# Performance work log

Measured on AMD Instinct MI355X. Metric: run time of the kernel, lower is better.

## Reference

```python
import jax, jax.numpy as jnp
import numpy as np
from functools import partial

P = 14          # patch size
IMG = 448       # image size
D = 1152        # hidden dim
H = 16          # num heads
DH = D // H     # head dim = 72
I = 4304        # intermediate dim
L = 4           # num layers
N = (IMG // P) ** 2  # 1024 patches
EPS = 1e-6


def setup_inputs() -> dict:
    key = jax.random.key(0)
    ks = jax.random.split(key, 24)
    s = 0.02
    inp = {
        "images": jax.random.normal(ks[0], (2, 2, IMG, IMG, 3), jnp.float32),
        "conv_w": jax.random.normal(ks[1], (P, P, 3, D), jnp.float32) * s,
        "conv_b": jnp.zeros((D,), jnp.float32),
        "pos_emb": jax.random.normal(ks[2], (N, D), jnp.float32) * s,
        # per-layer stacked parameters, leading axis L
        "ln1_g": jnp.ones((L, D), jnp.float32),
        "ln1_b": jnp.zeros((L, D), jnp.float32),
        "Wq": jax.random.normal(ks[3], (L, D, D), jnp.float32) * s,
        "bq": jnp.zeros((L, D), jnp.float32),
        "Wk": jax.random.normal(ks[4], (L, D, D), jnp.float32) * s,
        "bk": jnp.zeros((L, D), jnp.float32),
        "Wv": jax.random.normal(ks[5], (L, D, D), jnp.float32) * s,
        "bv": jnp.zeros((L, D), jnp.float32),
        "Wo": jax.random.normal(ks[6], (L, D, D), jnp.float32) * s,
        "bo": jnp.zeros((L, D), jnp.float32),
        "ln2_g": jnp.ones((L, D), jnp.float32),
        "ln2_b": jnp.zeros((L, D), jnp.float32),
        "W1": jax.random.normal(ks[7], (L, D, I), jnp.float32) * s,
        "b1": jnp.zeros((L, I), jnp.float32),
        "W2": jax.random.normal(ks[8], (L, I, D), jnp.float32) * s,
        "b2": jnp.zeros((L, D), jnp.float32),
        "lnf_g": jnp.ones((D,), jnp.float32),
        "lnf_b": jnp.zeros((D,), jnp.float32),
    }
    return inp


def _layernorm(x, g, b):
    mu = jnp.mean(x, axis=-1, keepdims=True)
    var = jnp.var(x, axis=-1, keepdims=True)
    return (x - mu) * jax.lax.rsqrt(var + EPS) * g + b


def _encoder(images, conv_w, conv_b, pos_emb, ln1_g, ln1_b, Wq, bq, Wk, bk,
             Wv, bv, Wo, bo, ln2_g, ln2_b, W1, b1, W2, b2, lnf_g, lnf_b):
    B, T = images.shape[0], images.shape[1]
    x = images.reshape((B * T,) + images.shape[2:])  # [BT, IMG, IMG, 3]
    # patch embedding: Conv2D stride=kernel=patch, VALID
    x = jax.lax.conv_general_dilated(
        x, conv_w, window_strides=(P, P), padding='VALID',
        dimension_numbers=('NHWC', 'HWIO', 'NHWC')) + conv_b
    x = x.reshape(B * T, N, D) + pos_emb  # add position embedding

    scale = 1.0 / jnp.sqrt(jnp.asarray(DH, x.dtype))

    def block(x, p):
        (g1, b1_, wq, bq_, wk, bk_, wv, bv_, wo, bo_, g2, b2_,
         w1, bm1, w2, bm2) = p
        h = _layernorm(x, g1, b1_)
        q = (h @ wq + bq_).reshape(-1, N, H, DH).transpose(0, 2, 1, 3)
        k = (h @ wk + bk_).reshape(-1, N, H, DH).transpose(0, 2, 1, 3)
        v = (h @ wv + bv_).reshape(-1, N, H, DH).transpose(0, 2, 1, 3)
        scores = jnp.einsum('bhqd,bhkd->bhqk', q, k) * scale
        probs = jax.nn.softmax(scores, axis=-1)
        attn = jnp.einsum('bhqk,bhkd->bhqd', probs, v)
        attn = attn.transpose(0, 2, 1, 3).reshape(-1, N, D)
        x = x + (attn @ wo + bo_)
        h = _layernorm(x, g2, b2_)
        h = jax.nn.gelu(h @ w1 + bm1, approximate=True) @ w2 + bm2
        return x + h, None

    params = (ln1_g, ln1_b, Wq, bq, Wk, bk, Wv, bv, Wo, bo,
              ln2_g, ln2_b, W1, b1, W2, b2)
    x, _ = jax.lax.scan(block, x, params)
    x = _layernorm(x, lnf_g, lnf_b)
    return x.reshape(B, T, N, D)


def reference(images, conv_w, conv_b, pos_emb, ln1_g, ln1_b, Wq, bq, Wk, bk,
              Wv, bv, Wo, bo, ln2_g, ln2_b, W1, b1, W2, b2, lnf_g, lnf_b):
    return _encoder(images, conv_w, conv_b, pos_emb, ln1_g, ln1_b, Wq, bq,
                    Wk, bk, Wv, bv, Wo, bo, ln2_g, ln2_b, W1, b1, W2, b2,
                    lnf_g, lnf_b)
```

## Files before the change

### kernel.cpp

```cpp
#include <hip/hip_runtime.h>
#include <hip/hip_bf16.h>
#include <stdint.h>
#include <math.h>

typedef __hip_bfloat16 bf16;
typedef __attribute__((ext_vector_type(4))) float floatx4;
typedef __attribute__((ext_vector_type(8))) __bf16 bf16x8;

typedef __attribute__((address_space(1))) void gvoid_t;
typedef __attribute__((address_space(3))) void lvoid_t;

__device__ __forceinline__ void gl_lds16(const void* g, void* l){
  __builtin_amdgcn_global_load_lds((gvoid_t*)g, (lvoid_t*)l, 16, 0, 0);
}

__device__ __forceinline__ float gelu_f(float v){
  float u = 0.7978845608028654f*(v + 0.044715f*v*v*v);
  float e = __expf(2.0f*u);
  return v*(1.0f - 1.0f/(e+1.0f));
}

template<int MODE>
__global__ __launch_bounds__(256,2)
void gemm_bf16(const bf16* __restrict__ A, const bf16* __restrict__ BT,
               const float* __restrict__ bias, void* __restrict__ C,
               int N, int K, int kc, float qs)
{
  __shared__ __align__(128) char ldsm[65536];
  const int tid  = threadIdx.x;
  const int wave = tid>>6, lane = tid&63;
  const int quad = lane>>4, l16 = lane&15;

  int bm, bn;
  {
    const int nx = gridDim.x;
    const int nwg = nx * gridDim.y;
    int lid = blockIdx.x + nx*blockIdx.y;
    const int q = nwg >> 3, r = nwg & 7;
    const int xcd = lid & 7, off = lid >> 3;
    lid = (xcd < r ? xcd*(q+1) : r*(q+1) + (xcd - r)*q) + off;
    const int per = nx << 3;
    const int g   = lid / per;
    const int rem = lid - g*per;
    bm = (g<<3) + (rem & 7);
    bn = rem >> 3;
  }
  const int m0 = bm*128, n0 = bn*128;

  const int s  = blockIdx.z;
  const int kb = s*kc;
  const int ke = min(K, kb + kc);
  const int T  = (ke - kb) >> 5;
  const int wm = (wave&1)*64, wn = (wave>>1)*64;
  floatx4 acc[4][4] = {};

  const int grow  = tid>>2;
  const int gslot = (tid&3) ^ (grow&3);
  const bf16* aBase = A  + (size_t)(m0 + grow)*K + kb + gslot*8;
  const bf16* bBase = BT + (size_t)(n0 + grow)*K + kb + gslot*8;
  const size_t rowK64 = (size_t)64*K;
  char* ldw = ldsm + (wave<<10);

  const int swz = (quad ^ (l16&3))<<4;
  const int aRd = ((wm + l16)<<6) + swz;
  const int bRd = ((wn + l16)<<6) + swz + 8192;

  auto stage = [&](int tp){
    char* ld = ldw + ((tp&3)<<14);
    const bf16* ga = aBase + (size_t)tp*32;
    const bf16* gb = bBase + (size_t)tp*32;
    gl_lds16(ga,          ld);
    gl_lds16(ga + rowK64, ld + 4096);
    gl_lds16(gb,          ld + 8192);
    gl_lds16(gb + rowK64, ld + 12288);
  };

  stage(0); stage(1); stage(2);

  for (int t=0; t<T; ++t){
    asm volatile("s_waitcnt vmcnt(8)" ::: "memory");
    asm volatile("s_barrier" ::: "memory");
    const char* bufb = ldsm + ((t&3)<<14);
    bf16x8 af[4], bfr[4];
#pragma unroll
    for (int i=0;i<4;i++) af[i]  = *(const bf16x8*)(bufb + aRd + (i<<10));
#pragma unroll
    for (int j=0;j<4;j++) bfr[j] = *(const bf16x8*)(bufb + bRd + (j<<10));
    stage(min(t+3, T-1));
    __builtin_amdgcn_s_setprio(1);
#pragma unroll
    for (int i=0;i<4;i++)
#pragma unroll
      for (int j=0;j<4;j++)
        acc[i][j] = __builtin_amdgcn_mfma_f32_16x16x32_bf16(af[i], bfr[j], acc[i][j], 0,0,0);
    __builtin_amdgcn_s_setprio(0);
  }
  asm volatile("s_waitcnt vmcnt(0)" ::: "memory");

  const float scale = (MODE==3 && n0<1152) ? qs : 1.0f;
#pragma unroll
  for (int i=0;i<4;i++){
    const int gr0 = m0 + wm + i*16 + quad*4;
#pragma unroll
    for (int j=0;j<4;j++){
      const int gc = n0 + wn + j*16 + l16;
      const float bv = (MODE!=4 || s==0) ? bias[gc] : 0.f;
#pragma unroll
      for (int r=0;r<4;r++){
        const int gr = gr0 + r;
        float v = acc[i][j][r] + bv;
        if constexpr (MODE==1) v = gelu_f(v);
        if constexpr (MODE==3) v *= scale;
        if constexpr (MODE==4){
          ((bf16*)C)[((size_t)s*4096 + gr)*N + gc] = __float2bfloat16(v);
        } else {
          ((bf16*)C)[(size_t)gr*N + gc] = __float2bfloat16(v);
        }
      }
    }
  }
}

template<int OUTF32, int WRITEX>
__global__ __launch_bounds__(256)
void ln_red(const float* __restrict__ base, unsigned bmask,
            const bf16* __restrict__ part, int ks,
            const float* __restrict__ g, const float* __restrict__ b,
            float* __restrict__ xw, void* __restrict__ out)
{
  const int row  = blockIdx.x*4 + (threadIdx.x>>6);
  const int lane = threadIdx.x & 63;
  const float2* br = (const float2*)base + (size_t)(row & bmask)*576;
  float2 v[9];
#pragma unroll
  for (int r=0;r<9;r++) v[r] = br[r*64+lane];
  for (int s=0;s<ks;s++){
    const __hip_bfloat162* pr = (const __hip_bfloat162*)part + ((size_t)s*4096 + row)*576;
#pragma unroll
    for (int r=0;r<9;r++){
      const float2 pv = __bfloat1622float2(pr[r*64+lane]);
      v[r].x += pv.x; v[r].y += pv.y;
    }
  }
  float sm=0.f, ss=0.f;
#pragma unroll
  for (int r=0;r<9;r++){
    sm += v[r].x + v[r].y;
    ss += v[r].x*v[r].x + v[r].y*v[r].y;
  }
#pragma unroll
  for (int m=1;m<64;m<<=1){ sm += __shfl_xor(sm,m,64); ss += __shfl_xor(ss,m,64); }
  const float mean = sm*(1.0f/1152.0f);
  const float rs = rsqrtf(ss*(1.0f/1152.0f) - mean*mean + 1e-6f);
  const float2* gr2 = (const float2*)g;
  const float2* br2 = (const float2*)b;
#pragma unroll
  for (int r=0;r<9;r++){
    const int c = r*64+lane;
    if constexpr (WRITEX) ((float2*)xw)[(size_t)row*576 + c] = v[r];
    const float2 gg = gr2[c], bb = br2[c];
    const float o0 = (v[r].x-mean)*rs*gg.x + bb.x;
    const float o1 = (v[r].y-mean)*rs*gg.y + bb.y;
    if constexpr (OUTF32){
      ((float2*)out)[(size_t)row*576 + c] = make_float2(o0, o1);
    } else {
      __hip_bfloat162 hv;
      hv.x = __float2bfloat16(o0); hv.y = __float2bfloat16(o1);
      ((__hip_bfloat162*)out)[(size_t)row*576 + c] = hv;
    }
  }
}

__global__ __launch_bounds__(256)
void im2col_kernel(const float* __restrict__ img, bf16* __restrict__ out)
{
  const int idx = blockIdx.x*256 + threadIdx.x;
  const int kk = idx % 608;
  const int rr = idx / 608;
  float v = 0.f;
  if (kk < 588){
    const int bt = rr >> 10, n = rr & 1023;
    const int py = n >> 5, px = n & 31;
    const int ph = kk / 42;
    const int rem = kk - ph*42;
    const int pw = rem / 3;
    const int c  = rem - pw*3;
    v = img[(((size_t)bt*448 + py*14 + ph)*448 + px*14 + pw)*3 + c];
  }
  out[idx] = __float2bfloat16(v);
}

__global__ __launch_bounds__(256)
void transpose_cvt(const float* __restrict__ in, bf16* __restrict__ out,
                   int K, int N, int Kp, int Np)
{
  __shared__ float tile[32][33];
  const int nt = blockIdx.x*32, kt = blockIdx.y*32;
  const int r = threadIdx.x>>5, c = threadIdx.x&31;
#pragma unroll
  for (int i=0;i<4;i++){
    const int k = kt + r + i*8, n = nt + c;
    tile[r+i*8][c] = (k<K && n<N) ? in[(size_t)k*N + n] : 0.f;
  }
  __syncthreads();
#pragma unroll
  for (int i=0;i<4;i++){
    const int n = nt + r + i*8, k = kt + c;
    out[(size_t)n*Kp + k] = __float2bfloat16(tile[c][r+i*8]);
  }
}

__global__ __launch_bounds__(256)
void pack_biases(const float* __restrict__ bq, const float* __restrict__ bk,
                 const float* __restrict__ bv, const float* __restrict__ b1,
                 int l, float* __restrict__ bqkv, float* __restrict__ b1p,
                 float4* __restrict__ zbuf)
{
  const int i = blockIdx.x*256 + threadIdx.x;
  if (i < 3456){
    float v;
    if (i < 1152)      v = bq[l*1152 + i];
    else if (i < 2304) v = bk[l*1152 + i - 1152];
    else               v = bv[l*1152 + i - 2304];
    bqkv[i] = v;
  }
  if (i < 4352) b1p[i] = (i < 4304) ? b1[l*4304 + i] : 0.f;
  if (i == 0) *zbuf = make_float4(0.f,0.f,0.f,0.f);
}

__global__ __launch_bounds__(256)
void transpose_v(const bf16* __restrict__ src, bf16* __restrict__ dst)
{
  __shared__ bf16 tile[128][73];
  const int nc = blockIdx.x, bh = blockIdx.y;
  const int bt = bh>>4, hh = bh&15;
  const bf16* s = src + ((size_t)bt*1024 + nc*128)*3456 + 2304 + hh*72;
  for (int e=threadIdx.x; e<128*72; e+=256){
    const int n = e/72, dh = e - n*72;
    tile[n][dh] = s[(size_t)n*3456 + dh];
  }
  __syncthreads();
  bf16* d = dst + (size_t)bh*80*1024 + nc*128;
  const bf16 z = __float2bfloat16(0.f);
  for (int e=threadIdx.x; e<80*128; e+=256){
    const int dh = e>>7, n = e&127;
    d[(size_t)dh*1024 + n] = (dh<72) ? tile[n][dh] : z;
  }
}

__global__ __launch_bounds__(256,2)
void attn_kernel(const bf16* __restrict__ qkv, const bf16* __restrict__ vb,
                 const float4* __restrict__ zbuf, bf16* __restrict__ outp)
{
  __shared__ bf16 Ks[128*96];
  __shared__ bf16 Vs[80*128];
  __shared__ bf16 Ps[64*128];
  const int tid = threadIdx.x, wave = tid>>6, lane = tid&63;
  const int quad = lane>>4, l16 = lane&15;
  int lid = blockIdx.x + (blockIdx.y<<4);
  lid = ((lid & 7) << 7) + (lid >> 3);
  const int bh = lid >> 4, q0 = (lid & 15) << 6;
  const int bt = bh>>4, hh = bh&15;
  const bf16* vg = vb + (size_t)bh*80*1024;
  bf16x8 af0{}, af1{}, af2{};
  {
    const bf16* qp = qkv + (size_t)(bt*1024 + q0 + wave*16 + l16)*3456 + hh*72 + quad*8;
    af0 = *(const bf16x8*)(qp);
    af1 = *(const bf16x8*)(qp+32);
    if (quad==0) af2 = *(const bf16x8*)(qp+64);
  }
  float mr[4], lr[4];
#pragma unroll
  for (int r=0;r<4;r++){ mr[r] = -3.0e38f; lr[r] = 0.f; }
  floatx4 oacc[5] = {};
  for (int kc=0;kc<8;kc++){
    __syncthreads();
    {
      const char* kcb = (const char*)(qkv + (size_t)(bt*1024 + kc*128)*3456 + 1152 + hh*72);
#pragma unroll
      for (int i=0;i<6;i++){
        const int u = (wave*6+i)*64 + lane;
        const int row = u/12;
        const int pp = u - row*12;
        const int c = (pp & 12) | ((pp & 3) ^ (row & 3));
        const void* src = (c<9) ? (const void*)(kcb + (size_t)row*6912 + c*16)
                                : (const void*)zbuf;
        gl_lds16(src, (char*)Ks + (size_t)(wave*6+i)*1024);
      }
#pragma unroll
      for (int i=0;i<5;i++){
        const int u = (wave*5+i)*64 + lane;
        const int row = u>>4;
        const int pp = u & 15;
        const int c = (pp & 8) | ((pp & 7) ^ (row & 7));
        gl_lds16((const char*)vg + (size_t)row*2048 + kc*256 + c*16,
                 (char*)Vs + (size_t)(wave*5+i)*1024);
      }
    }
    __syncthreads();
    floatx4 sc[8] = {};
    const int ksw = (quad ^ (l16&3))*8;
#pragma unroll
    for (int ct=0;ct<8;ct++){
      const bf16* kr = Ks + (ct*16+l16)*96 + ksw;
      sc[ct] = __builtin_amdgcn_mfma_f32_16x16x32_bf16(af0, *(const bf16x8*)(kr   ), sc[ct],0,0,0);
      sc[ct] = __builtin_amdgcn_mfma_f32_16x16x32_bf16(af1, *(const bf16x8*)(kr+32), sc[ct],0,0,0);
      sc[ct] = __builtin_amdgcn_mfma_f32_16x16x32_bf16(af2, *(const bf16x8*)(kr+64), sc[ct],0,0,0);
    }
    float cm[4];
#pragma unroll
    for (int r=0;r<4;r++){
      cm[r] = sc[0][r];
#pragma unroll
      for (int ct=1;ct<8;ct++) cm[r] = fmaxf(cm[r], sc[ct][r]);
    }
#pragma unroll
    for (int off=1; off<16; off<<=1)
#pragma unroll
      for (int r=0;r<4;r++) cm[r] = fmaxf(cm[r], __shfl_xor(cm[r], off, 64));
    float al[4], ls[4];
#pragma unroll
    for (int r=0;r<4;r++){
      const float mn = fmaxf(mr[r], cm[r]);
      al[r] = exp2f(mr[r]-mn);
      mr[r] = mn; ls[r] = 0.f;
    }
#pragma unroll
    for (int ct=0;ct<8;ct++){
#pragma unroll
      for (int r=0;r<4;r++){
        const float pv = exp2f(sc[ct][r]-mr[r]);
        ls[r] += pv;
        const int row = wave*16+quad*4+r;
        const int c = ct*2 + (l16>>3);
        const int pp = (c & 8) | ((c & 7) ^ (row & 7));
        Ps[row*128 + pp*8 + (l16&7)] = __float2bfloat16(pv);
      }
    }
#pragma unroll
    for (int off=1; off<16; off<<=1)
#pragma unroll
      for (int r=0;r<4;r++) ls[r] += __shfl_xor(ls[r], off, 64);
#pragma unroll
    for (int r=0;r<4;r++) lr[r] = lr[r]*al[r] + ls[r];
#pragma unroll
    for (int t=0;t<5;t++)
#pragma unroll
      for (int r=0;r<4;r++) oacc[t][r] *= al[r];
    __syncthreads();
#pragma unroll
    for (int ks=0;ks<4;ks++){
      const int c = ks*4 + quad;
      const int pp = (c & 8) | ((c & 7) ^ (l16 & 7));
      const bf16x8 pf = *(const bf16x8*)(Ps + (wave*16+l16)*128 + pp*8);
#pragma unroll
      for (int t=0;t<5;t++){
        const bf16x8 vf = *(const bf16x8*)(Vs + (t*16+l16)*128 + pp*8);
        oacc[t] = __builtin_amdgcn_mfma_f32_16x16x32_bf16(pf, vf, oacc[t],0,0,0);
      }
    }
  }
#pragma unroll
  for (int t=0;t<5;t++){
    const int dh = t*16+l16;
    if (dh < 72){
#pragma unroll
      for (int r=0;r<4;r++){
        const int q = wave*16 + quad*4 + r;
        const float v = oacc[t][r] / lr[r];
        outp[((size_t)bt*1024 + q0 + q)*1152 + hh*72 + dh] = __float2bfloat16(v);
      }
    }
  }
}

extern "C" void kernel_launch(void* const* d_in, const int* in_sizes, int n_in,
                              void* d_out, int out_size, void* d_ws, size_t ws_size,
                              hipStream_t stream)
{
  (void)in_sizes; (void)n_in; (void)out_size; (void)ws_size;
  const float* images = (const float*)d_in[0];
  const float* conv_w = (const float*)d_in[1];
  const float* conv_b = (const float*)d_in[2];
  const float* pos_emb= (const float*)d_in[3];
  const float* ln1_g  = (const float*)d_in[4];
  const float* ln1_b  = (const float*)d_in[5];
  const float* Wq     = (const float*)d_in[6];
  const float* bq     = (const float*)d_in[7];
  const float* Wk     = (const float*)d_in[8];
  const float* bk     = (const float*)d_in[9];
  const float* Wv     = (const float*)d_in[10];
  const float* bv     = (const float*)d_in[11];
  const float* Wo     = (const float*)d_in[12];
  const float* bo     = (const float*)d_in[13];
  const float* ln2_g  = (const float*)d_in[14];
  const float* ln2_b  = (const float*)d_in[15];
  const float* W1     = (const float*)d_in[16];
  const float* b1     = (const float*)d_in[17];
  const float* W2     = (const float*)d_in[18];
  const float* b2     = (const float*)d_in[19];
  const float* lnf_g  = (const float*)d_in[20];
  const float* lnf_b  = (const float*)d_in[21];

  char* p = (char*)d_ws;
  auto take = [&](size_t nbytes)->char*{ char* q = p; p += (nbytes + 255) & ~(size_t)255; return q; };
  float* xw   = (float*)take(4096ull*1152*4);
  bf16* hbuf  = (bf16*) take(4096ull*1152*2);
  bf16* h1    = (bf16*) take(4096ull*4352*2);
  bf16* qkvr  = h1;
  bf16* vbuf  = (bf16*) take(64ull*80*1024*2);
  bf16* imcol = vbuf;
  bf16* aout  = (bf16*) take(4096ull*1152*2);
  bf16* WqkvT = (bf16*) take(3456ull*1152*2);
  bf16* WoT   = (bf16*) take(1152ull*1152*2);
  bf16* W1T   = (bf16*) take(4352ull*1152*2);
  bf16* cwT   = W1T;
  bf16* W2T   = (bf16*) take(1152ull*4352*2);
  bf16* Ppart = (bf16*) take(4ull*4096*1152*2);
  float* bqkv = (float*)take(3456*4);
  float* b1p  = (float*)take(4352*4);
  float4* zbuf= (float4*)take(256);

  const float qscale = 1.4426950408889634f / sqrtf(72.0f);

  im2col_kernel<<<9728, 256, 0, stream>>>(images, imcol);
  transpose_cvt<<<dim3(36,19), 256, 0, stream>>>(conv_w, cwT, 588, 1152, 608, 1152);
  gemm_bf16<4><<<dim3(9,32,2), 256, 0, stream>>>(imcol, cwT, conv_b, Ppart, 1152, 608, 320, 0.f);

  for (int l=0;l<4;l++){
    transpose_cvt<<<dim3(36,36), 256, 0, stream>>>(Wq + (size_t)l*1152*1152, WqkvT,                1152,1152,1152,1152);
    transpose_cvt<<<dim3(36,36), 256, 0, stream>>>(Wk + (size_t)l*1152*1152, WqkvT + 1152ull*1152, 1152,1152,1152,1152);
    transpose_cvt<<<dim3(36,36), 256, 0, stream>>>(Wv + (size_t)l*1152*1152, WqkvT + 2304ull*1152, 1152,1152,1152,1152);
    transpose_cvt<<<dim3(36,36), 256, 0, stream>>>(Wo + (size_t)l*1152*1152, WoT, 1152,1152,1152,1152);
    transpose_cvt<<<dim3(136,36),256, 0, stream>>>(W1 + (size_t)l*1152*4304, W1T, 1152,4304,1152,4352);
    transpose_cvt<<<dim3(36,136),256, 0, stream>>>(W2 + (size_t)l*4304*1152, W2T, 4304,1152,4352,1152);
    pack_biases<<<17,256,0,stream>>>(bq,bk,bv,b1,l,bqkv,b1p,zbuf);

    if (l==0)
      ln_red<0,1><<<1024,256,0,stream>>>(pos_emb, 1023u, Ppart, 2, ln1_g, ln1_b, xw, hbuf);
    else
      ln_red<0,1><<<1024,256,0,stream>>>(xw, 4095u, Ppart, 4, ln1_g + l*1152, ln1_b + l*1152, xw, hbuf);

    gemm_bf16<3><<<dim3(27,32,1),256,0,stream>>>(hbuf, WqkvT, bqkv, qkvr, 3456, 1152, 1152, qscale);
    transpose_v<<<dim3(8,64),256,0,stream>>>(qkvr, vbuf);
    attn_kernel<<<dim3(16,64),256,0,stream>>>(qkvr, vbuf, zbuf, aout);
    gemm_bf16<4><<<dim3(9,32,3),256,0,stream>>>(aout, WoT, bo + l*1152, Ppart, 1152, 1152, 384, 0.f);
    ln_red<0,1><<<1024,256,0,stream>>>(xw, 4095u, Ppart, 3, ln2_g + l*1152, ln2_b + l*1152, xw, hbuf);

    gemm_bf16<1><<<dim3(34,32,1),256,0,stream>>>(hbuf, W1T, b1p, h1, 4352, 1152, 1152, 0.f);
    gemm_bf16<4><<<dim3(9,32,4),256,0,stream>>>(h1, W2T, b2 + l*1152, Ppart, 1152, 4352, 1088, 0.f);
  }
  ln_red<1,0><<<1024,256,0,stream>>>(xw, 4095u, Ppart, 4, lnf_g, lnf_b, nullptr, (float*)d_out);
}
```

Before: 1.636 ms.

## Restructure attention softmax with lazy rescale, ones-column row sums, and LDS reuse

The attention kernel now computes scores transposed, so each lane owns one query row. It rescales the output accumulator only when the running max grows by more than a threshold. The row sum is obtained from an extra all-ones column appended to V (dh==72) instead of shuffle reductions. P is written into the Ks buffer instead of a separate Ps array, which reduces LDS use and allows three blocks per CU. The GEMM pipeline drops redundant tail stage loads and uses tail-aware waitcnt values. The lazy rescale stores probabilities relative to a stale max, which can reach 2^8 in bf16 and is a precision risk.

```diff
diff --git a/kernel.cpp b/kernel.cpp
--- a/kernel.cpp
+++ b/kernel.cpp
@@ -6,6 +6,7 @@
 typedef __hip_bfloat16 bf16;
 typedef __attribute__((ext_vector_type(4))) float floatx4;
 typedef __attribute__((ext_vector_type(8))) __bf16 bf16x8;
+typedef __attribute__((ext_vector_type(4))) __bf16 bf16x4;
 
 typedef __attribute__((address_space(1))) void gvoid_t;
 typedef __attribute__((address_space(3))) void lvoid_t;
@@ -78,7 +79,10 @@
   stage(0); stage(1); stage(2);
 
   for (int t=0; t<T; ++t){
-    asm volatile("s_waitcnt vmcnt(8)" ::: "memory");
+    const int rem = T-1-t;
+    if (rem >= 2)      asm volatile("s_waitcnt vmcnt(8)" ::: "memory");
+    else if (rem == 1) asm volatile("s_waitcnt vmcnt(4)" ::: "memory");
+    else               asm volatile("s_waitcnt vmcnt(0)" ::: "memory");
     asm volatile("s_barrier" ::: "memory");
     const char* bufb = ldsm + ((t&3)<<14);
     bf16x8 af[4], bfr[4];
@@ -86,7 +90,7 @@
     for (int i=0;i<4;i++) af[i]  = *(const bf16x8*)(bufb + aRd + (i<<10));
 #pragma unroll
     for (int j=0;j<4;j++) bfr[j] = *(const bf16x8*)(bufb + bRd + (j<<10));
-    stage(min(t+3, T-1));
+    if (t+3 < T) stage(t+3);
     __builtin_amdgcn_s_setprio(1);
 #pragma unroll
     for (int i=0;i<4;i++)
@@ -95,7 +99,6 @@
         acc[i][j] = __builtin_amdgcn_mfma_f32_16x16x32_bf16(af[i], bfr[j], acc[i][j], 0,0,0);
     __builtin_amdgcn_s_setprio(0);
   }
-  asm volatile("s_waitcnt vmcnt(0)" ::: "memory");
 
   const float scale = (MODE==3 && n0<1152) ? qs : 1.0f;
 #pragma unroll
@@ -241,20 +244,20 @@
   }
   __syncthreads();
   bf16* d = dst + (size_t)bh*80*1024 + nc*128;
-  const bf16 z = __float2bfloat16(0.f);
+  const bf16 z  = __float2bfloat16(0.f);
+  const bf16 on = __float2bfloat16(1.f);
   for (int e=threadIdx.x; e<80*128; e+=256){
     const int dh = e>>7, n = e&127;
-    d[(size_t)dh*1024 + n] = (dh<72) ? tile[n][dh] : z;
-  }
-}
-
-__global__ __launch_bounds__(256,2)
+    d[(size_t)dh*1024 + n] = (dh<72) ? tile[n][dh] : (dh==72 ? on : z);
+  }
+}
+
+__global__ __launch_bounds__(256,3)
 void attn_kernel(const bf16* __restrict__ qkv, const bf16* __restrict__ vb,
                  const float4* __restrict__ zbuf, bf16* __restrict__ outp)
 {
   __shared__ bf16 Ks[128*96];
   __shared__ bf16 Vs[80*128];
-  __shared__ bf16 Ps[64*128];
   const int tid = threadIdx.x, wave = tid>>6, lane = tid&63;
   const int quad = lane>>4, l16 = lane&15;
   int lid = blockIdx.x + (blockIdx.y<<4);
@@ -269,10 +272,12 @@
     af1 = *(const bf16x8*)(qp+32);
     if (quad==0) af2 = *(const bf16x8*)(qp+64);
   }
-  float mr[4], lr[4];
-#pragma unroll
-  for (int r=0;r<4;r++){ mr[r] = -3.0e38f; lr[r] = 0.f; }
+  float mr = -3.0e38f;
   floatx4 oacc[5] = {};
+  const int prow = wave*16 + l16;
+  const int hi2 = (l16>>2)&3, lo2 = l16&3;
+  char* const psrow = (char*)Ks + prow*256;
+
   for (int kc=0;kc<8;kc++){
     __syncthreads();
     {
@@ -303,56 +308,50 @@
 #pragma unroll
     for (int ct=0;ct<8;ct++){
       const bf16* kr = Ks + (ct*16+l16)*96 + ksw;
-      sc[ct] = __builtin_amdgcn_mfma_f32_16x16x32_bf16(af0, *(const bf16x8*)(kr   ), sc[ct],0,0,0);
-      sc[ct] = __builtin_amdgcn_mfma_f32_16x16x32_bf16(af1, *(const bf16x8*)(kr+32), sc[ct],0,0,0);
-      sc[ct] = __builtin_amdgcn_mfma_f32_16x16x32_bf16(af2, *(const bf16x8*)(kr+64), sc[ct],0,0,0);
-    }
-    float cm[4];
-#pragma unroll
-    for (int r=0;r<4;r++){
-      cm[r] = sc[0][r];
-#pragma unroll
-      for (int ct=1;ct<8;ct++) cm[r] = fmaxf(cm[r], sc[ct][r]);
-    }
-#pragma unroll
-    for (int off=1; off<16; off<<=1)
-#pragma unroll
-      for (int r=0;r<4;r++) cm[r] = fmaxf(cm[r], __shfl_xor(cm[r], off, 64));
-    float al[4], ls[4];
-#pragma unroll
-    for (int r=0;r<4;r++){
-      const float mn = fmaxf(mr[r], cm[r]);
-      al[r] = exp2f(mr[r]-mn);
-      mr[r] = mn; ls[r] = 0.f;
-    }
+      sc[ct] = __builtin_amdgcn_mfma_f32_16x16x32_bf16(*(const bf16x8*)(kr   ), af0, sc[ct],0,0,0);
+      sc[ct] = __builtin_amdgcn_mfma_f32_16x16x32_bf16(*(const bf16x8*)(kr+32), af1, sc[ct],0,0,0);
+      sc[ct] = __builtin_amdgcn_mfma_f32_16x16x32_bf16(*(const bf16x8*)(kr+64), af2, sc[ct],0,0,0);
+    }
+    float cm = sc[0][0];
+#pragma unroll
+    for (int ct=0;ct<8;ct++)
+#pragma unroll
+      for (int r=0;r<4;r++) cm = fmaxf(cm, sc[ct][r]);
+    cm = fmaxf(cm, __shfl_xor(cm, 16, 64));
+    cm = fmaxf(cm, __shfl_xor(cm, 32, 64));
+    if (!__all(cm <= mr + 8.0f)){
+      const float mn = fmaxf(mr, cm);
+      const float alv = exp2f(mr - mn);
+      mr = mn;
+      float alb[4];
+#pragma unroll
+      for (int r=0;r<4;r++) alb[r] = __shfl(alv, quad*4 + r, 64);
+#pragma unroll
+      for (int t=0;t<5;t++)
+#pragma unroll
+        for (int r=0;r<4;r++) oacc[t][r] *= alb[r];
+    }
+    __syncthreads();
 #pragma unroll
     for (int ct=0;ct<8;ct++){
-#pragma unroll
-      for (int r=0;r<4;r++){
-        const float pv = exp2f(sc[ct][r]-mr[r]);
-        ls[r] += pv;
-        const int row = wave*16+quad*4+r;
-        const int c = ct*2 + (l16>>3);
-        const int pp = (c & 8) | ((c & 7) ^ (row & 7));
-        Ps[row*128 + pp*8 + (l16&7)] = __float2bfloat16(pv);
-      }
-    }
-#pragma unroll
-    for (int off=1; off<16; off<<=1)
-#pragma unroll
-      for (int r=0;r<4;r++) ls[r] += __shfl_xor(ls[r], off, 64);
-#pragma unroll
-    for (int r=0;r<4;r++) lr[r] = lr[r]*al[r] + ls[r];
-#pragma unroll
-    for (int t=0;t<5;t++)
-#pragma unroll
-      for (int r=0;r<4;r++) oacc[t][r] *= al[r];
-    __syncthreads();
+      bf16x4 pk;
+      pk[0] = (__bf16)exp2f(sc[ct][0] - mr);
+      pk[1] = (__bf16)exp2f(sc[ct][1] - mr);
+      pk[2] = (__bf16)exp2f(sc[ct][2] - mr);
+      pk[3] = (__bf16)exp2f(sc[ct][3] - mr);
+      *(bf16x4*)(psrow + (((ct^hi2)<<5) | ((quad^lo2)<<3))) = pk;
+    }
 #pragma unroll
     for (int ks=0;ks<4;ks++){
+      const int ct0 = 2*ks + (quad>>1);
+      const int g0 = (quad&1)*2;
+      const bf16x4 plo = *(const bf16x4*)(psrow + (((ct0^hi2)<<5) | (((g0  )^lo2)<<3)));
+      const bf16x4 phi = *(const bf16x4*)(psrow + (((ct0^hi2)<<5) | (((g0+1)^lo2)<<3)));
+      bf16x8 pf;
+      pf[0]=plo[0]; pf[1]=plo[1]; pf[2]=plo[2]; pf[3]=plo[3];
+      pf[4]=phi[0]; pf[5]=phi[1]; pf[6]=phi[2]; pf[7]=phi[3];
       const int c = ks*4 + quad;
       const int pp = (c & 8) | ((c & 7) ^ (l16 & 7));
-      const bf16x8 pf = *(const bf16x8*)(Ps + (wave*16+l16)*128 + pp*8);
 #pragma unroll
       for (int t=0;t<5;t++){
         const bf16x8 vf = *(const bf16x8*)(Vs + (t*16+l16)*128 + pp*8);
@@ -360,6 +359,12 @@
       }
     }
   }
+  float inv[4];
+#pragma unroll
+  for (int r=0;r<4;r++){
+    const float lr = __shfl(oacc[4][r], quad*16 + 8, 64);
+    inv[r] = 1.0f / lr;
+  }
 #pragma unroll
   for (int t=0;t<5;t++){
     const int dh = t*16+l16;
@@ -367,7 +372,7 @@
 #pragma unroll
       for (int r=0;r<4;r++){
         const int q = wave*16 + quad*4 + r;
-        const float v = oacc[t][r] / lr[r];
+        const float v = oacc[t][r] * inv[r];
         outp[((size_t)bt*1024 + q0 + q)*1152 + hh*72 + dh] = __float2bfloat16(v);
       }
     }
```

Measured after the change: 1.553 ms. -5.1%, faster.
